# Performance work log

Measured on AMD Instinct MI355X. Metric: run time of the kernel, lower is better.

## Reference

```python
import jax, jax.numpy as jnp
import numpy as np

N0, N1, N2, N3 = 8192, 32768, 65536, 65536
CUM = (N0, N0 + N1, N0 + N1 + N2, N0 + N1 + N2 + N3)  # nodes through hop k
NTOT = CUM[3]
EH = (131072, 262144, 262144)                          # edges per hop (per edge type)
ECUM = (EH[0], EH[0] + EH[1], EH[0] + EH[1] + EH[2])
ETOT = ECUM[2]
C, H, T = 64, 256, 3
HH = H // 2
B, L = 16, 512  # N0 == B * L: equal-length note sequences per graph
LN_EPS = 1e-5


def _ln(x, w, b):
    m = x.mean(-1, keepdims=True)
    v = x.var(-1, keepdims=True)
    return (x - m) / jnp.sqrt(v + LN_EPS) * w + b


def _seg_mean(msgs, dst, n):
    s = jax.ops.segment_sum(msgs, dst, num_segments=n)
    cnt = jax.ops.segment_sum(jnp.ones(dst.shape, msgs.dtype), dst, num_segments=n)
    return s / jnp.maximum(cnt, 1.0)[:, None]


def _l2(x):
    return x / jnp.maximum(jnp.linalg.norm(x, axis=-1, keepdims=True), 1e-12)


def _gru_dir(x, wih, whh, bih, bhh, reverse):
    # x: [B, Lt, Din]; torch gate order (r, z, n)
    gi = jnp.einsum('bld,gd->blg', x, wih) + bih
    gi = jnp.moveaxis(gi, 1, 0)  # [Lt, B, 3*HH]
    h0 = jnp.zeros((x.shape[0], HH), x.dtype)

    def step(h, g):
        gh = h @ whh.T + bhh
        ir, iz, in_ = jnp.split(g, 3, -1)
        hr, hz, hn = jnp.split(gh, 3, -1)
        r = jax.nn.sigmoid(ir + hr)
        z = jax.nn.sigmoid(iz + hz)
        n = jnp.tanh(in_ + r * hn)
        hnew = (1.0 - z) * n + z * h
        return hnew, hnew

    _, ys = jax.lax.scan(step, h0, gi, reverse=reverse)
    return jnp.moveaxis(ys, 0, 1)  # [B, Lt, HH]


def _bigru(x, wih, whh, bih, bhh):
    f = _gru_dir(x, wih[0], whh[0], bih[0], bhh[0], False)
    bwd = _gru_dir(x, wih[1], whh[1], bih[1], bhh[1], True)
    return jnp.concatenate([f, bwd], -1)


def _forward(x, edge_index, batch_size, sage0_proj_w, sage0_proj_b, sage0_lw, sage0_lb,
             sage0_rw, sage_lw, sage_lb, sage_rw, ln_w, ln_b,
             gru_wih0, gru_whh0, gru_bih0, gru_bhh0,
             gru_wih1, gru_whh1, gru_bih1, gru_bhh1,
             rnn_norm_w, rnn_norm_b, mlp1_w, mlp1_b, mlp_ln_w, mlp_ln_b,
             mlp2_w, mlp2_b, cat_w, cat_b):
    # ---- hybrid GRU branch on seed notes (equal lengths -> pad == reshape) ----
    xs = x[:batch_size].reshape(B, L, C)
    h = _bigru(xs, gru_wih0, gru_whh0, gru_bih0, gru_bhh0)
    h = _bigru(h, gru_wih1, gru_whh1, gru_bih1, gru_bhh1)  # inter-layer dropout: eval mode
    h = _ln(h, rnn_norm_w, rnn_norm_b)
    h = _ln(jax.nn.relu(h @ mlp1_w + mlp1_b), mlp_ln_w, mlp_ln_b) @ mlp2_w + mlp2_b
    x_rnn = h.reshape(batch_size, H)

    # ---- GNN layer 0: SAGEConv(project=True, normalize=True), hetero mean over T types ----
    feat = x
    outs = []
    for t in range(T):
        src, dst = edge_index[t, 0], edge_index[t, 1]
        xp = jax.nn.relu(feat @ sage0_proj_w[t] + sage0_proj_b[t])
        agg = _seg_mean(xp[src], dst, NTOT)
        outs.append(_l2(agg @ sage0_lw[t] + sage0_lb[t] + feat @ sage0_rw[t]))
    feat = sum(outs) / T
    feat = _ln(jax.nn.relu(feat), ln_w[0], ln_b[0])  # dropout: eval mode (identity)

    # ---- layers 1..2 with trim_to_layer: drop last sampled hop each layer ----
    n_layer = (CUM[2], CUM[1])
    e_layer = (ECUM[1], ECUM[0])
    for i in range(2):
        n, e = n_layer[i], e_layer[i]
        feat = feat[:n]
        outs = []
        for t in range(T):
            src, dst = edge_index[t, 0, :e], edge_index[t, 1, :e]
            agg = _seg_mean(feat[src], dst, n)
            outs.append(agg @ sage_lw[i, t] + sage_lb[i, t] + feat @ sage_rw[i, t])
        feat = sum(outs) / T
        if i == 0:
            feat = _ln(jax.nn.relu(feat), ln_w[1], ln_b[1])
    x_gnn = feat[:batch_size]
    return jnp.concatenate([x_rnn, x_gnn], -1) @ cat_w + cat_b


def setup_inputs():
    key = jax.random.key(0)
    ks = iter(jax.random.split(key, 64))

    def nrm(shape, fan_in):
        return jax.random.normal(next(ks), shape, jnp.float32) / float(np.sqrt(fan_in))

    # hop-structured edges: hop k has src < CUM[k+1], dst < CUM[k]
    ei = []
    for t in range(T):
        rows, cols = [], []
        for k in range(3):
            rows.append(jax.random.randint(next(ks), (EH[k],), 0, CUM[k + 1]))
            cols.append(jax.random.randint(next(ks), (EH[k],), 0, CUM[k]))
        ei.append(jnp.stack([jnp.concatenate(rows), jnp.concatenate(cols)]))
    edge_index = jnp.stack(ei).astype(jnp.int32)

    return dict(
        x=jax.random.normal(next(ks), (NTOT, C), jnp.float32),
        edge_index=edge_index,
        batch=(jnp.arange(N0) // L).astype(jnp.int32),
        batch_size=N0,
        sage0_proj_w=nrm((T, C, C), C), sage0_proj_b=jnp.zeros((T, C), jnp.float32),
        sage0_lw=nrm((T, C, H), C), sage0_lb=jnp.zeros((T, H), jnp.float32),
        sage0_rw=nrm((T, C, H), C),
        sage_lw=nrm((2, T, H, H), H), sage_lb=jnp.zeros((2, T, H), jnp.float32),
        sage_rw=nrm((2, T, H, H), H),
        ln_w=jnp.ones((2, H), jnp.float32), ln_b=jnp.zeros((2, H), jnp.float32),
        gru_wih0=nrm((2, 3 * HH, C), C), gru_whh0=nrm((2, 3 * HH, HH), HH),
        gru_bih0=jnp.zeros((2, 3 * HH), jnp.float32), gru_bhh0=jnp.zeros((2, 3 * HH), jnp.float32),
        gru_wih1=nrm((2, 3 * HH, H), H), gru_whh1=nrm((2, 3 * HH, HH), HH),
        gru_bih1=jnp.zeros((2, 3 * HH), jnp.float32), gru_bhh1=jnp.zeros((2, 3 * HH), jnp.float32),
        rnn_norm_w=jnp.ones((H,), jnp.float32), rnn_norm_b=jnp.zeros((H,), jnp.float32),
        mlp1_w=nrm((H, H), H), mlp1_b=jnp.zeros((H,), jnp.float32),
        mlp_ln_w=jnp.ones((H,), jnp.float32), mlp_ln_b=jnp.zeros((H,), jnp.float32),
        mlp2_w=nrm((H, H), H), mlp2_b=jnp.zeros((H,), jnp.float32),
        cat_w=nrm((2 * H, H), 2 * H), cat_b=jnp.zeros((H,), jnp.float32),
    )


def reference(x, edge_index, batch, batch_size, sage0_proj_w, sage0_proj_b, sage0_lw,
              sage0_lb, sage0_rw, sage_lw, sage_lb, sage_rw, ln_w, ln_b,
              gru_wih0, gru_whh0, gru_bih0, gru_bhh0, gru_wih1, gru_whh1, gru_bih1,
              gru_bhh1, rnn_norm_w, rnn_norm_b, mlp1_w, mlp1_b, mlp_ln_w, mlp_ln_b,
              mlp2_w, mlp2_b, cat_w, cat_b):
    # batch encodes 16 equal-length (512) sequences; bincount/pad == reshape above
    return _forward(x, edge_index, batch_size, sage0_proj_w, sage0_proj_b, sage0_lw,
                    sage0_lb, sage0_rw, sage_lw, sage_lb, sage_rw, ln_w, ln_b,
                    gru_wih0, gru_whh0, gru_bih0, gru_bhh0, gru_wih1, gru_whh1,
                    gru_bih1, gru_bhh1, rnn_norm_w, rnn_norm_b, mlp1_w, mlp1_b,
                    mlp_ln_w, mlp_ln_b, mlp2_w, mlp2_b, cat_w, cat_b)
```

## Files before the change

kernel.cpp:

```cpp
#include <hip/hip_runtime.h>
#include <stdint.h>

typedef unsigned short u16;
typedef __attribute__((ext_vector_type(8))) short short8;
typedef __attribute__((ext_vector_type(4))) short short4v;
typedef __attribute__((ext_vector_type(4))) float float4v;

#define DEV static __device__ __forceinline__

DEV float bf2f(u16 u){ union { unsigned int i; float f; } c; c.i = ((unsigned int)u) << 16; return c.f; }
DEV u16 f2bf(float f){ union { float ff; unsigned int i; } c; c.ff = f;
  unsigned int x = c.i; return (u16)((x + 0x7fffu + ((x >> 16) & 1u)) >> 16); }

#define MFMA16(a,b,c) __builtin_amdgcn_mfma_f32_16x16x32_bf16((a),(b),(c),0,0,0)

#define ETOTC  655360
#define TSTRIDE 155648
#define NBINS   466944

__global__ void detect_dtype(const u16* __restrict__ xs, int* __restrict__ flag){
  __shared__ int sh[256];
  int t = threadIdx.x; int cnt = 0;
  for (int i = t; i < 4096; i += 256){
    u16 u = xs[i]; int e = (u >> 7) & 0xff;
    cnt += (u == 0 || (e >= 112 && e <= 143)) ? 1 : 0;
  }
  sh[t] = cnt; __syncthreads();
  for (int d = 128; d; d >>= 1){ if (t < d) sh[t] += sh[t+d]; __syncthreads(); }
  if (t == 0) flag[0] = (sh[0] >= 3686) ? 1 : 0;
}

DEV u16 scrub(u16 v){ int e = (v >> 7) & 0xff; return (e == 0xff) ? (u16)0 : v; }

__global__ void convert_x(const void* __restrict__ xin, const int* __restrict__ flag,
                          u16* __restrict__ out){
  int i = blockIdx.x*256 + threadIdx.x;
  u16 v[4];
  if (flag[0] == 1){
    short4v s = ((const short4v*)xin)[i];
#pragma unroll
    for (int j=0;j<4;j++) v[j] = scrub((u16)s[j]);
  } else {
    float4v f = ((const float4v*)xin)[i];
#pragma unroll
    for (int j=0;j<4;j++) v[j] = scrub(f2bf(f[j]));
  }
  short4v o; o[0]=(short)v[0]; o[1]=(short)v[1]; o[2]=(short)v[2]; o[3]=(short)v[3];
  ((short4v*)out)[i] = o;
}

struct WSrc { const void* p[28]; };
__device__ const int g_wcum[29] = {0,12288,12480,61632,62400,111552,504768,506304,899520,
  900032,900544,949696,1048000,1048768,1049536,1246144,1344448,1345216,1345984,1346240,
  1346496,1412032,1412288,1412544,1412800,1478336,1478592,1609664,1609920};

__global__ void convert_w(WSrc d, const int* __restrict__ flag, u16* __restrict__ out){
  int i = blockIdx.x*256 + threadIdx.x;
  if (i >= 1609920) return;
  int lo = 0, hi = 28;
  while (hi - lo > 1){ int m = (lo+hi) >> 1; if (i >= g_wcum[m]) lo = m; else hi = m; }
  int off = i - g_wcum[lo];
  u16 v = (flag[0] == 1) ? ((const u16*)d.p[lo])[off]
                         : f2bf(((const float*)d.p[lo])[off]);
  out[i] = scrub(v);
}

__global__ void packT(const u16* __restrict__ in, u16* __restrict__ out, int K, int N){
  int i = blockIdx.x*256 + threadIdx.x;
  if (i < K*N){ int n = i / K, k = i - n*K; out[i] = in[(size_t)k*N + n]; }
}

__global__ void pack_lr(const u16* __restrict__ lw, const u16* __restrict__ rw,
                        u16* __restrict__ out, int F){
  int K2 = 2*F; long total = 3L*256*K2;
  long i = (long)blockIdx.x*256 + threadIdx.x;
  if (i < total){
    int k = (int)(i % K2); int n = (int)((i / K2) & 255); int t = (int)(i / ((long)K2*256));
    out[i] = (k < F) ? lw[((size_t)t*F + k)*256 + n]
                     : rw[((size_t)t*F + (k-F))*256 + n];
  }
}

__global__ void hist3(const int* __restrict__ ei, int* __restrict__ cnt){
  int g = blockIdx.x*256 + threadIdx.x;
  int t = g / ETOTC, e = g - t*ETOTC;
  int dst = ei[(size_t)t*2*ETOTC + ETOTC + e];
  int base = t*TSTRIDE;
  atomicAdd(&cnt[base + dst], 1);
  if (e < 393216) atomicAdd(&cnt[base + 106496 + dst], 1);
  if (e < 131072) atomicAdd(&cnt[base + 147456 + dst], 1);
}

__global__ void perm3(const int* __restrict__ ei, const int* __restrict__ off,
                      int* __restrict__ slot, int* __restrict__ srcs){
  int g = blockIdx.x*256 + threadIdx.x;
  int t = g / ETOTC, e = g - t*ETOTC;
  int dst = ei[(size_t)t*2*ETOTC + ETOTC + e];
  int src = ei[(size_t)t*2*ETOTC + e];
  int base = t*TSTRIDE;
  { int b = base + dst; srcs[off[b] + atomicAdd(&slot[b], 1)] = src; }
  if (e < 393216){ int b = base + 106496 + dst;
    srcs[off[b] + atomicAdd(&slot[b], 1)] = src; }
  if (e < 131072){ int b = base + 147456 + dst;
    srcs[off[b] + atomicAdd(&slot[b], 1)] = src; }
}

__global__ void scan_blocks(const int* __restrict__ cnt, int* __restrict__ off,
                            int* __restrict__ bsum, int n){
  __shared__ int sh[256];
  int t = threadIdx.x;
  int base = blockIdx.x*2048 + t*8;
  int v[8]; int tot = 0;
#pragma unroll
  for (int j=0;j<8;j++){ v[j] = (base+j < n) ? cnt[base+j] : 0; tot += v[j]; }
  sh[t] = tot; __syncthreads();
  for (int d=1; d<256; d<<=1){
    int y = (t>=d) ? sh[t-d] : 0; __syncthreads();
    sh[t] += y; __syncthreads();
  }
  int run = sh[t] - tot;
#pragma unroll
  for (int j=0;j<8;j++){ if (base+j < n) off[base+j] = run; run += v[j]; }
  if (t == 255) bsum[blockIdx.x] = sh[255];
}

__global__ void scan_top(int* __restrict__ bsum, int G){
  __shared__ int sh[256];
  int t = threadIdx.x;
  int v = (t < G) ? bsum[t] : 0;
  sh[t] = v; __syncthreads();
  for (int d=1; d<256; d<<=1){
    int y = (t>=d) ? sh[t-d] : 0; __syncthreads();
    sh[t] += y; __syncthreads();
  }
  if (t < G) bsum[t] = sh[t] - v;
}

__global__ void scan_add(int* __restrict__ off, const int* __restrict__ bsum, int n){
  int add = bsum[blockIdx.x];
  int base = blockIdx.x*2048 + threadIdx.x*8;
#pragma unroll
  for (int j=0;j<8;j++) if (base+j < n) off[base+j] += add;
}

template<int F>
DEV void gather_body(int w, int lane,
    const int* __restrict__ off, const int* __restrict__ cnt, const int* __restrict__ srcs,
    const u16* __restrict__ feat, int ld, u16* __restrict__ out)
{
  int st = off[w], c = cnt[w];
  float sc = 1.f / (float)(c < 1 ? 1 : c);
  if (F == 64) {
    float a = 0.f, b = 0.f;
    int i = 0;
    for (; i + 4 <= c; i += 4){
      int s0 = srcs[st+i], s1 = srcs[st+i+1], s2 = srcs[st+i+2], s3 = srcs[st+i+3];
      u16 u0 = feat[(size_t)s0*ld + lane];
      u16 u1 = feat[(size_t)s1*ld + lane];
      u16 u2 = feat[(size_t)s2*ld + lane];
      u16 u3 = feat[(size_t)s3*ld + lane];
      a += bf2f(u0) + bf2f(u1);
      b += bf2f(u2) + bf2f(u3);
    }
    for (; i < c; ++i){ int s = srcs[st+i]; a += bf2f(feat[(size_t)s*ld + lane]); }
    out[(size_t)w*64 + lane] = f2bf((a + b)*sc);
  } else {
    float a0=0.f,a1=0.f,a2=0.f,a3=0.f;
    float b0=0.f,b1=0.f,b2=0.f,b3=0.f;
    int i = 0;
    for (; i + 4 <= c; i += 4){
      int s0 = srcs[st+i], s1 = srcs[st+i+1], s2 = srcs[st+i+2], s3 = srcs[st+i+3];
      short4v u0 = *(const short4v*)(feat + (size_t)s0*ld + lane*4);
      short4v u1 = *(const short4v*)(feat + (size_t)s1*ld + lane*4);
      short4v u2 = *(const short4v*)(feat + (size_t)s2*ld + lane*4);
      short4v u3 = *(const short4v*)(feat + (size_t)s3*ld + lane*4);
      a0 += bf2f((u16)u0[0]) + bf2f((u16)u1[0]);
      a1 += bf2f((u16)u0[1]) + bf2f((u16)u1[1]);
      a2 += bf2f((u16)u0[2]) + bf2f((u16)u1[2]);
      a3 += bf2f((u16)u0[3]) + bf2f((u16)u1[3]);
      b0 += bf2f((u16)u2[0]) + bf2f((u16)u3[0]);
      b1 += bf2f((u16)u2[1]) + bf2f((u16)u3[1]);
      b2 += bf2f((u16)u2[2]) + bf2f((u16)u3[2]);
      b3 += bf2f((u16)u2[3]) + bf2f((u16)u3[3]);
    }
    for (; i < c; ++i){
      int s = srcs[st+i];
      short4v u = *(const short4v*)(feat + (size_t)s*ld + lane*4);
      a0 += bf2f((u16)u[0]); a1 += bf2f((u16)u[1]);
      a2 += bf2f((u16)u[2]); a3 += bf2f((u16)u[3]);
    }
    u16* o = out + (size_t)w*256 + lane*4;
    o[0]=f2bf((a0+b0)*sc); o[1]=f2bf((a1+b1)*sc);
    o[2]=f2bf((a2+b2)*sc); o[3]=f2bf((a3+b3)*sc);
  }
}

template<int F>
__global__ __launch_bounds__(256,4) void gather_mean(
    const int* __restrict__ off, const int* __restrict__ cnt, const int* __restrict__ srcs,
    const u16* __restrict__ feat, int ld, u16* __restrict__ out, int rows)
{
  int w = blockIdx.x*4 + (threadIdx.x >> 6);
  int lane = threadIdx.x & 63;
  if (w >= rows) return;
  gather_body<F>(w, lane, off, cnt, srcs, feat, ld, out);
}

__global__ __launch_bounds__(256,2) void ln_rows(
    const u16* __restrict__ in, u16* __restrict__ out,
    const u16* __restrict__ w, const u16* __restrict__ b, int rows)
{
  int r = blockIdx.x*4 + (threadIdx.x >> 6);
  int lane = threadIdx.x & 63;
  if (r >= rows) return;
  short4v u = *(const short4v*)(in + (size_t)r*256 + lane*4);
  float v[4];
#pragma unroll
  for (int i=0;i<4;i++) v[i] = bf2f((u16)u[i]);
  float s = v[0]+v[1]+v[2]+v[3];
  float q = v[0]*v[0]+v[1]*v[1]+v[2]*v[2]+v[3]*v[3];
#pragma unroll
  for (int d=1; d<64; d<<=1){ s += __shfl_xor(s, d); q += __shfl_xor(q, d); }
  float mu = s * (1.f/256.f);
  float var = fmaxf(q * (1.f/256.f) - mu*mu, 0.f);
  float rs = rsqrtf(var + 1e-5f);
  u16* o = out + (size_t)r*256 + lane*4;
#pragma unroll
  for (int i=0;i<4;i++){
    int col = lane*4 + i;
    o[i] = f2bf((v[i]-mu)*rs*bf2f(w[col]) + bf2f(b[col]));
  }
}

#define LGKM0_SB do{ asm volatile("s_waitcnt lgkmcnt(0)" ::: "memory"); \
                     __builtin_amdgcn_sched_barrier(0); \
                     __builtin_amdgcn_s_barrier(); \
                     __builtin_amdgcn_sched_barrier(0); }while(0)

#define GRU_STEP(S, C0, C1, C2) do{                                          \
    const int l_ = dir ? (511 - (S)) : (S);                                  \
    short8 afr_[4];                                                          \
    _Pragma("unroll")                                                        \
    for (int kt=0; kt<4; kt++) afr_[kt] = *(const short8*)(&hbf[kt*32 + lg*8]); \
    float4v acc_[4];                                                         \
    _Pragma("unroll")                                                        \
    for (int nt=0; nt<4; nt++) acc_[nt] = (float4v){0.f,0.f,0.f,0.f};        \
    _Pragma("unroll")                                                        \
    for (int kt=0; kt<4; kt++){                                              \
      _Pragma("unroll")                                                      \
      for (int nt=0; nt<4; nt++) acc_[nt] = MFMA16(afr_[kt], bfrag[nt][kt], acc_[nt]); } \
    if (lane < 16){                                                          \
      _Pragma("unroll")                                                      \
      for (int nt=0; nt<4; nt++) ghs[64*w + nt*16 + lane] = acc_[nt][0];     \
    }                                                                        \
    LGKM0_SB;                                                                \
    if (tid < 128){                                                          \
      float ghr = ghs[tid]       + bhr;                                      \
      float ghz = ghs[128 + tid] + bhz;                                      \
      float ghn = ghs[256 + tid] + bhn;                                      \
      float r_ = 1.f/(1.f + __expf(-((C0) + ghr)));                          \
      float z_ = 1.f/(1.f + __expf(-((C1) + ghz)));                          \
      float xn_ = (C2) + r_*ghn;                                             \
      float th_ = 1.f - 2.f/(__expf(2.f*xn_) + 1.f);                         \
      hreg = (1.f - z_)*th_ + z_*hreg;                                       \
      u16 hb_ = f2bf(hreg);                                                  \
      hbf[tid] = hb_;                                                        \
      hout[((size_t)(b*512 + l_))*256 + dir*128 + tid] = hb_;                \
      int sn_ = (S) + 2;                                                     \
      if (sn_ < 512){                                                        \
        int ln2_ = dir ? (511 - sn_) : sn_;                                  \
        const float* g_ = gbase + (size_t)ln2_*768;                          \
        (C0) = g_[0]; (C1) = g_[128]; (C2) = g_[256];                        \
      }                                                                      \
    }                                                                        \
    LGKM0_SB;                                                                \
  }while(0)

DEV void gru_body(const float* __restrict__ gi, const u16* __restrict__ whh,
                  const u16* __restrict__ bhh, u16* __restrict__ hout,
                  int bid, u16* hbf, float* ghs)
{
  const int b = bid >> 1, dir = bid & 1;
  const int tid = threadIdx.x;
  const int w = tid >> 6, lane = tid & 63;
  const int lr = lane & 15, lg = lane >> 4;

  short8 bfrag[4][4];
#pragma unroll
  for (int nt=0; nt<4; nt++)
#pragma unroll
    for (int kt=0; kt<4; kt++){
      int n = 64*w + nt*16 + lr;
      bfrag[nt][kt] = *(const short8*)(whh + ((size_t)(dir*384 + n))*128 + kt*32 + lg*8);
    }

  const float* gbase = gi + (size_t)b*512*768 + dir*384 + tid;
  float hreg = 0.f, bhr = 0.f, bhz = 0.f, bhn = 0.f;
  float a0=0.f,a1=0.f,a2=0.f, e0=0.f,e1=0.f,e2=0.f;
  if (tid < 128){
    bhr = bf2f(bhh[dir*384 + tid]);
    bhz = bf2f(bhh[dir*384 + 128 + tid]);
    bhn = bf2f(bhh[dir*384 + 256 + tid]);
    const float* g0 = gbase + (size_t)(dir ? 511 : 0)*768;
    a0 = g0[0]; a1 = g0[128]; a2 = g0[256];
    const float* g1 = gbase + (size_t)(dir ? 510 : 1)*768;
    e0 = g1[0]; e1 = g1[128]; e2 = g1[256];
  }
  if (tid < 64) ((unsigned int*)hbf)[tid] = 0u;
  LGKM0_SB;

  for (int s2 = 0; s2 < 512; s2 += 2){
    GRU_STEP(s2,     a0, a1, a2);
    GRU_STEP(s2 + 1, e0, e1, e2);
  }
}

template<int F>
__global__ __launch_bounds__(384,1) void fused_gru_gather(
    const float* __restrict__ gi, const u16* __restrict__ whh,
    const u16* __restrict__ bhh, u16* __restrict__ hout,
    const int* __restrict__ off0, const int* __restrict__ cnt0, const int* __restrict__ srcs,
    const u16* __restrict__ feat, int ld, int featstep,
    u16* __restrict__ aggout, long aggstride, int rows, int bpt)
{
  __shared__ u16 hbf[128];
  __shared__ float ghs[384];
  if (blockIdx.x < 32){
    gru_body(gi, whh, bhh, hout, blockIdx.x, hbf, ghs);
    return;
  }
  int gb = blockIdx.x - 32;
  int t = gb / bpt, rb = gb - t*bpt;
  int w = rb*6 + (threadIdx.x >> 6);
  int lane = threadIdx.x & 63;
  if (w >= rows) return;
  gather_body<F>(w, lane, off0 + t*TSTRIDE, cnt0 + t*TSTRIDE, srcs,
                 feat + (size_t)t*featstep, ld, aggout + (size_t)t*aggstride);
}

template<int EPI, bool OUTF32>
__global__ __launch_bounds__(256,1) void gemm_bt(
    const u16* __restrict__ A, int lda,
    const u16* __restrict__ WT, int K, int N,
    const u16* __restrict__ bias,
    const u16* __restrict__ lnw, const u16* __restrict__ lnb,
    void* __restrict__ Cp, int ldc, const int* __restrict__ dynof)
{
  __shared__ u16 As[64*72];
  __shared__ u16 Bs[256*72];
  __shared__ float redS[4][64];
  __shared__ float redQ[4][64];
  __shared__ float muL[64], rsL[64];
  const int tid = threadIdx.x;
  const int lane = tid & 63, wid = tid >> 6;
  const int lr = lane & 15, lg = lane >> 4;
  const int m0 = blockIdx.x * 64;
  const int col0 = blockIdx.y * 256;
  float4v acc[4][4];
#pragma unroll
  for (int i=0;i<4;i++)
#pragma unroll
    for (int j=0;j<4;j++) acc[i][j] = (float4v){0.f,0.f,0.f,0.f};

  for (int k0 = 0; k0 < K; k0 += 64){
#pragma unroll
    for (int v = 0; v < 2; v++){
      int idx = tid + v*256; int r = idx >> 3, c8 = (idx & 7) << 3;
      *(short8*)(&As[r*72 + c8]) = *(const short8*)(A + (size_t)(m0+r)*lda + k0 + c8);
    }
#pragma unroll
    for (int v = 0; v < 8; v++){
      int idx = tid + v*256; int nn = idx >> 3, c8 = (idx & 7) << 3;
      short8 val = {0,0,0,0,0,0,0,0};
      if (col0 + nn < N) val = *(const short8*)(WT + (size_t)(col0+nn)*K + k0 + c8);
      *(short8*)(&Bs[nn*72 + c8]) = val;
    }
    __syncthreads();
#pragma unroll
    for (int kk = 0; kk < 2; kk++){
      short8 af[4], bfr[4];
#pragma unroll
      for (int i=0;i<4;i++) af[i]  = *(const short8*)(&As[(16*i+lr)*72 + kk*32 + lg*8]);
#pragma unroll
      for (int j=0;j<4;j++) bfr[j] = *(const short8*)(&Bs[(wid*64+16*j+lr)*72 + kk*32 + lg*8]);
#pragma unroll
      for (int i=0;i<4;i++)
#pragma unroll
        for (int j=0;j<4;j++) acc[i][j] = MFMA16(af[i], bfr[j], acc[i][j]);
    }
    __syncthreads();
  }
  int cols[4];
#pragma unroll
  for (int j=0;j<4;j++) cols[j] = col0 + wid*64 + 16*j + lr;
#pragma unroll
  for (int j=0;j<4;j++){
    float bv = (cols[j] < N) ? bf2f(bias[cols[j]]) : 0.f;
#pragma unroll
    for (int i=0;i<4;i++)
#pragma unroll
      for (int r=0;r<4;r++) acc[i][j][r] += bv;
  }
  if (EPI >= 1){
#pragma unroll
    for (int i=0;i<4;i++)
#pragma unroll
      for (int j=0;j<4;j++)
#pragma unroll
        for (int r=0;r<4;r++) acc[i][j][r] = fmaxf(acc[i][j][r], 0.f);
  }
  if (EPI == 2){
#pragma unroll
    for (int i=0;i<4;i++)
#pragma unroll
      for (int r=0;r<4;r++){
        float p = acc[i][0][r]+acc[i][1][r]+acc[i][2][r]+acc[i][3][r];
        float q = acc[i][0][r]*acc[i][0][r]+acc[i][1][r]*acc[i][1][r]
                 +acc[i][2][r]*acc[i][2][r]+acc[i][3][r]*acc[i][3][r];
#pragma unroll
        for (int d=1; d<16; d<<=1){ p += __shfl_xor(p,d); q += __shfl_xor(q,d); }
        if (lr == 0){ redS[wid][16*i + lg*4 + r] = p; redQ[wid][16*i + lg*4 + r] = q; }
      }
    __syncthreads();
    if (tid < 64){
      float s = redS[0][tid]+redS[1][tid]+redS[2][tid]+redS[3][tid];
      float q = redQ[0][tid]+redQ[1][tid]+redQ[2][tid]+redQ[3][tid];
      float mu = s * (1.f/256.f);
      float var = fmaxf(q * (1.f/256.f) - mu*mu, 0.f);
      muL[tid] = mu; rsL[tid] = rsqrtf(var + 1e-5f);
    }
    __syncthreads();
#pragma unroll
    for (int i=0;i<4;i++)
#pragma unroll
      for (int r=0;r<4;r++){
        int rl = 16*i + lg*4 + r;
        float mu = muL[rl], rs = rsL[rl];
#pragma unroll
        for (int j=0;j<4;j++){
          float w = bf2f(lnw[cols[j]]), bb = bf2f(lnb[cols[j]]);
          acc[i][j][r] = (acc[i][j][r]-mu)*rs*w + bb;
        }
      }
  }
  bool of32 = OUTF32;
  if (dynof) of32 = (dynof[0] == 0);
#pragma unroll
  for (int i=0;i<4;i++)
#pragma unroll
    for (int r=0;r<4;r++){
      int row = m0 + 16*i + lg*4 + r;
#pragma unroll
      for (int j=0;j<4;j++) if (cols[j] < N){
        if (of32) ((float*)Cp)[(size_t)row*ldc + cols[j]] = acc[i][j][r];
        else ((u16*)Cp)[(size_t)row*ldc + cols[j]] = f2bf(acc[i][j][r]);
      }
    }
}

template<int F, bool DO_L2, bool DO_LN>
__global__ __launch_bounds__(256,1) void sage_fused(
    const u16* __restrict__ A1, long a1t, const u16* __restrict__ A2, int lda2,
    const u16* __restrict__ WTp, const u16* __restrict__ lbp,
    const u16* __restrict__ lnw, const u16* __restrict__ lnb,
    u16* __restrict__ out, int ldc, int outcol)
{
  constexpr int K2 = 2*F;
  __shared__ u16 As[64*72];
  __shared__ u16 Bs[256*72];
  __shared__ float redS[4][64];
  __shared__ float redQ[4][64];
  __shared__ float rowA[64], rowB[64];
  const int tid = threadIdx.x;
  const int lane = tid & 63, wid = tid >> 6;
  const int lr = lane & 15, lg = lane >> 4;
  const int m0 = blockIdx.x * 64;
  int colsL[4];
#pragma unroll
  for (int j=0;j<4;j++) colsL[j] = wid*64 + 16*j + lr;
  float4v facc[4][4];
#pragma unroll
  for (int i=0;i<4;i++)
#pragma unroll
    for (int j=0;j<4;j++) facc[i][j] = (float4v){0.f,0.f,0.f,0.f};

  for (int t=0; t<3; ++t){
    float4v acc[4][4];
#pragma unroll
    for (int i=0;i<4;i++)
#pragma unroll
      for (int j=0;j<4;j++) acc[i][j] = (float4v){0.f,0.f,0.f,0.f};
    const u16* WT  = WTp + (size_t)t*256*K2;
    const u16* A1b = A1 + (size_t)t*a1t;
    for (int k0 = 0; k0 < K2; k0 += 64){
      const u16* Ab; int la, kb;
      if (k0 < F){ Ab = A1b; la = F; kb = k0; } else { Ab = A2; la = lda2; kb = k0 - F; }
#pragma unroll
      for (int v=0; v<2; v++){
        int idx = tid + v*256; int r = idx >> 3, c8 = (idx & 7) << 3;
        *(short8*)(&As[r*72 + c8]) = *(const short8*)(Ab + (size_t)(m0+r)*la + kb + c8);
      }
#pragma unroll
      for (int v=0; v<8; v++){
        int idx = tid + v*256; int nn = idx >> 3, c8 = (idx & 7) << 3;
        *(short8*)(&Bs[nn*72 + c8]) = *(const short8*)(WT + (size_t)nn*K2 + k0 + c8);
      }
      __syncthreads();
#pragma unroll
      for (int kk = 0; kk < 2; kk++){
        short8 af[4], bfr[4];
#pragma unroll
        for (int i=0;i<4;i++) af[i]  = *(const short8*)(&As[(16*i+lr)*72 + kk*32 + lg*8]);
#pragma unroll
        for (int j=0;j<4;j++) bfr[j] = *(const short8*)(&Bs[(wid*64+16*j+lr)*72 + kk*32 + lg*8]);
#pragma unroll
        for (int i=0;i<4;i++)
#pragma unroll
          for (int j=0;j<4;j++) acc[i][j] = MFMA16(af[i], bfr[j], acc[i][j]);
      }
      __syncthreads();
    }
#pragma unroll
    for (int j=0;j<4;j++){
      float bv = bf2f(lbp[t*256 + colsL[j]]);
#pragma unroll
      for (int i=0;i<4;i++)
#pragma unroll
        for (int r=0;r<4;r++) acc[i][j][r] += bv;
    }
    if (DO_L2){
#pragma unroll
      for (int i=0;i<4;i++)
#pragma unroll
        for (int r=0;r<4;r++){
          float q = acc[i][0][r]*acc[i][0][r]+acc[i][1][r]*acc[i][1][r]
                   +acc[i][2][r]*acc[i][2][r]+acc[i][3][r]*acc[i][3][r];
#pragma unroll
          for (int d=1; d<16; d<<=1) q += __shfl_xor(q,d);
          if (lr == 0) redQ[wid][16*i + lg*4 + r] = q;
        }
      __syncthreads();
      if (tid < 64){
        float q = redQ[0][tid]+redQ[1][tid]+redQ[2][tid]+redQ[3][tid];
        rowA[tid] = 1.f / fmaxf(sqrtf(q), 1e-12f);
      }
      __syncthreads();
#pragma unroll
      for (int i=0;i<4;i++)
#pragma unroll
        for (int r=0;r<4;r++){
          float sc = rowA[16*i + lg*4 + r];
#pragma unroll
          for (int j=0;j<4;j++) acc[i][j][r] *= sc;
        }
      __syncthreads();
    }
#pragma unroll
    for (int i=0;i<4;i++)
#pragma unroll
      for (int j=0;j<4;j++)
#pragma unroll
        for (int r=0;r<4;r++) facc[i][j][r] += acc[i][j][r];
  }
  const float inv3 = (1.f/3.f);
#pragma unroll
  for (int i=0;i<4;i++)
#pragma unroll
    for (int j=0;j<4;j++)
#pragma unroll
      for (int r=0;r<4;r++) facc[i][j][r] *= inv3;
  if (DO_LN){
#pragma unroll
    for (int i=0;i<4;i++)
#pragma unroll
      for (int j=0;j<4;j++)
#pragma unroll
        for (int r=0;r<4;r++) facc[i][j][r] = fmaxf(facc[i][j][r], 0.f);
#pragma unroll
    for (int i=0;i<4;i++)
#pragma unroll
      for (int r=0;r<4;r++){
        float p = facc[i][0][r]+facc[i][1][r]+facc[i][2][r]+facc[i][3][r];
        float q = facc[i][0][r]*facc[i][0][r]+facc[i][1][r]*facc[i][1][r]
                 +facc[i][2][r]*facc[i][2][r]+facc[i][3][r]*facc[i][3][r];
#pragma unroll
        for (int d=1; d<16; d<<=1){ p += __shfl_xor(p,d); q += __shfl_xor(q,d); }
        if (lr == 0){ redS[wid][16*i + lg*4 + r] = p; redQ[wid][16*i + lg*4 + r] = q; }
      }
    __syncthreads();
    if (tid < 64){
      float s = redS[0][tid]+redS[1][tid]+redS[2][tid]+redS[3][tid];
      float q = redQ[0][tid]+redQ[1][tid]+redQ[2][tid]+redQ[3][tid];
      float mu = s * (1.f/256.f);
      float var = fmaxf(q * (1.f/256.f) - mu*mu, 0.f);
      rowA[tid] = mu; rowB[tid] = rsqrtf(var + 1e-5f);
    }
    __syncthreads();
#pragma unroll
    for (int i=0;i<4;i++)
#pragma unroll
      for (int r=0;r<4;r++){
        int rl = 16*i + lg*4 + r;
        float mu = rowA[rl], rs = rowB[rl];
#pragma unroll
        for (int j=0;j<4;j++){
          float w = bf2f(lnw[colsL[j]]), bb = bf2f(lnb[colsL[j]]);
          facc[i][j][r] = (facc[i][j][r]-mu)*rs*w + bb;
        }
      }
  }
#pragma unroll
  for (int i=0;i<4;i++)
#pragma unroll
    for (int r=0;r<4;r++){
      int row = m0 + 16*i + lg*4 + r;
#pragma unroll
      for (int j=0;j<4;j++)
        out[(size_t)row*ldc + outcol + colsL[j]] = f2bf(facc[i][j][r]);
    }
}

extern "C" void kernel_launch(void* const* d_in, const int* in_sizes, int n_in,
                              void* d_out, int out_size, void* d_ws, size_t ws_size,
                              hipStream_t stream)
{
  (void)in_sizes; (void)n_in; (void)out_size;
  const int* ei = (const int*)d_in[1];

  char* ws = (char*)d_ws;
  size_t o = 0;
  auto alloc = [&](size_t b){ size_t p = o; o += (b + 255) & ~(size_t)255; return p; };
  char* RA   = ws + alloc(66060288);
  u16* XP3   = (u16*)RA;
  u16* AGGB1 = (u16*)RA;
  char* RR   = ws + alloc(41943040);
  float* GI  = (float*)RR;
  u16* H0    = (u16*)(RR + 25165824);
  u16* H1    = (u16*)(RR + 29360128);
  u16* HA    = (u16*)(RR + 33554432);
  u16* HB    = (u16*)(RR + 37748736);
  char* RB   = ws + alloc(40894464);
  u16* AGGB0 = (u16*)RB;
  u16* AGGB2 = (u16*)RB;
  u16* FEAT2 = (u16*)(RB + 12582912);
  u16* FEAT  = (u16*)(ws + alloc(106496ull*256*2));
  u16* CAT   = (u16*)(ws + alloc(8192ull*512*2));
  u16* AR    = (u16*)(ws + alloc(12619968ull*2));
  u16* WXP   = (u16*)(ws + alloc(192ull*64*2));
  u16* WP0   = (u16*)(ws + alloc(3ull*256*128*2));
  u16* WP1   = (u16*)(ws + alloc(3ull*256*512*2));
  u16* WP2   = (u16*)(ws + alloc(3ull*256*512*2));
  u16* M1T   = (u16*)(ws + alloc(256ull*256*2));
  u16* M2T   = (u16*)(ws + alloc(256ull*256*2));
  u16* CTT   = (u16*)(ws + alloc(256ull*512*2));
  int* CNT   = (int*)(ws + alloc((size_t)NBINS*4));
  int* OFF   = (int*)(ws + alloc((size_t)NBINS*4));
  int* SLOT  = (int*)(ws + alloc((size_t)NBINS*4));
  int* BSUM  = (int*)(ws + alloc(256ull*4));
  int* SRCS  = (int*)(ws + alloc(3538944ull*4));
  int* FLAG  = (int*)(ws + alloc(256));
  if (o > ws_size) return;

  u16* x16    = AR;
  u16* projw6 = AR + 11010048; u16* projb6 = AR + 11022336;
  u16* s0lw6  = AR + 11022528; u16* s0lb6  = AR + 11071680; u16* s0rw6 = AR + 11072448;
  u16* slw6   = AR + 11121600; u16* slb6   = AR + 11514816; u16* srw6  = AR + 11516352;
  u16* lnw6   = AR + 11909568; u16* lnb6   = AR + 11910080;
  u16* wih0b  = AR + 11910592; u16* whh0b  = AR + 11959744;
  u16* bih0b  = AR + 12058048; u16* bhh0b  = AR + 12058816;
  u16* wih1b  = AR + 12059584; u16* whh1b  = AR + 12256192;
  u16* bih1b  = AR + 12354496; u16* bhh1b  = AR + 12355264;
  u16* rnw6   = AR + 12356032; u16* rnb6   = AR + 12356288;
  u16* mlp1w6 = AR + 12356544; u16* mlp1b6 = AR + 12422080;
  u16* mlnw6  = AR + 12422336; u16* mlnb6  = AR + 12422592;
  u16* mlp2w6 = AR + 12422848; u16* mlp2b6 = AR + 12488384;
  u16* catw6  = AR + 12488640; u16* catb6  = AR + 12619712;

  detect_dtype<<<dim3(1),dim3(256),0,stream>>>((const u16*)d_in[0], FLAG);
  convert_x<<<dim3(10752),dim3(256),0,stream>>>(d_in[0], FLAG, x16);
  WSrc wsrc;
  for (int i=0;i<28;i++) wsrc.p[i] = d_in[4+i];
  convert_w<<<dim3(6289),dim3(256),0,stream>>>(wsrc, FLAG, AR + 11010048);

  packT<<<dim3(256),dim3(256),0,stream>>>(mlp1w6, M1T, 256, 256);
  packT<<<dim3(256),dim3(256),0,stream>>>(mlp2w6, M2T, 256, 256);
  packT<<<dim3(512),dim3(256),0,stream>>>(catw6,  CTT, 512, 256);
  for (int t=0;t<3;t++)
    packT<<<dim3(16),dim3(256),0,stream>>>(projw6 + (size_t)t*4096, WXP + (size_t)t*4096, 64, 64);
  pack_lr<<<dim3(384),dim3(256),0,stream>>>(s0lw6, s0rw6, WP0, 64);
  pack_lr<<<dim3(1536),dim3(256),0,stream>>>(slw6,               srw6,               WP1, 256);
  pack_lr<<<dim3(1536),dim3(256),0,stream>>>(slw6 + 3ull*256*256, srw6 + 3ull*256*256, WP2, 256);

  hipMemsetAsync(CNT, 0, (size_t)NBINS*4, stream);
  hist3<<<dim3(7680),dim3(256),0,stream>>>(ei, CNT);
  scan_blocks<<<dim3(228),dim3(256),0,stream>>>(CNT, OFF, BSUM, NBINS);
  scan_top<<<dim3(1),dim3(256),0,stream>>>(BSUM, 228);
  scan_add<<<dim3(228),dim3(256),0,stream>>>(OFF, BSUM, NBINS);
  hipMemsetAsync(SLOT, 0, (size_t)NBINS*4, stream);
  perm3<<<dim3(7680),dim3(256),0,stream>>>(ei, OFF, SLOT, SRCS);

  gemm_bt<0,true><<<dim3(128,3),dim3(256),0,stream>>>(x16, 64, wih0b, 64, 768, bih0b, nullptr, nullptr, GI, 768, nullptr);
  gemm_bt<1,false><<<dim3(2688,1),dim3(256),0,stream>>>(x16, 64, WXP, 64, 192, projb6, nullptr, nullptr, XP3, 192, nullptr);

  fused_gru_gather<64><<<dim3(32 + 3*17750),dim3(384),0,stream>>>(
      GI, whh0b, bhh0b, H0,
      OFF, CNT, SRCS, XP3, 192, 64, AGGB0, (long)106496*64, 106496, 17750);

  gemm_bt<0,true><<<dim3(128,3),dim3(256),0,stream>>>(H0, 256, wih1b, 256, 768, bih1b, nullptr, nullptr, GI, 768, nullptr);
  sage_fused<64,true,true><<<dim3(1664),dim3(256),0,stream>>>(
      AGGB0, (long)106496*64, x16, 64, WP0, s0lb6, lnw6, lnb6, FEAT, 256, 0);

  fused_gru_gather<256><<<dim3(32 + 3*6827),dim3(384),0,stream>>>(
      GI, whh1b, bhh1b, H1,
      OFF + 106496, CNT + 106496, SRCS, FEAT, 256, 0, AGGB1, (long)40960*256, 40960, 6827);

  sage_fused<256,false,true><<<dim3(640),dim3(256),0,stream>>>(
      AGGB1, (long)40960*256, FEAT, 256, WP1, slb6, lnw6+256, lnb6+256, FEAT2, 256, 0);
  for (int t=0;t<3;t++)
    gather_mean<256><<<dim3(2048),dim3(256),0,stream>>>(
        OFF + t*TSTRIDE + 147456, CNT + t*TSTRIDE + 147456, SRCS, FEAT2, 256,
        AGGB2 + (size_t)t*8192*256, 8192);
  sage_fused<256,false,false><<<dim3(128),dim3(256),0,stream>>>(
      AGGB2, (long)8192*256, FEAT2, 256, WP2, slb6 + 3*256, nullptr, nullptr, CAT, 512, 256);

  ln_rows<<<dim3(2048),dim3(256),0,stream>>>(H1, HA, rnw6, rnb6, 8192);
  gemm_bt<2,false><<<dim3(128,1),dim3(256),0,stream>>>(HA, 256, M1T, 256, 256, mlp1b6, mlnw6, mlnb6, HB, 256, nullptr);
  gemm_bt<0,false><<<dim3(128,1),dim3(256),0,stream>>>(HB, 256, M2T, 256, 256, mlp2b6, nullptr, nullptr, CAT, 512, nullptr);

  gemm_bt<0,false><<<dim3(128,1),dim3(256),0,stream>>>(CAT, 512, CTT, 512, 256, catb6,
      nullptr, nullptr, d_out, 256, FLAG);
}
```

Before: 1.526 ms.

## Merge independent GEMM, SAGE, LN and gather launches into horizontally fused kernels

Independent stages (GRU input GEMM with SAGE layer 0, SAGE layer 1 with the RNN LayerNorm, MLP1 with the layer-2 gathers, MLP2 with SAGE layer 2) are combined into single launches that pick their role from the block index, using one shared-memory struct. This is meant to cut launch overhead and fill the GPU with concurrent work from independent branches. It also raises the GRU recurrence wave priority so co-resident gather blocks do not delay the serial critical path. The risks are that gather and LN blocks now run under the 256-thread, 1-block launch bounds and reserve the full GEMM shared memory, which may lower their occupancy.

```diff
diff --git a/kernel.cpp b/kernel.cpp
--- a/kernel.cpp
+++ b/kernel.cpp
@@ -17,6 +17,14 @@
 #define ETOTC  655360
 #define TSTRIDE 155648
 #define NBINS   466944
+
+struct SM {
+  u16 As[64*72];
+  u16 Bs[256*72];
+  float redS[4][64];
+  float redQ[4][64];
+  float rowA[64], rowB[64];
+};
 
 __global__ void detect_dtype(const u16* __restrict__ xs, int* __restrict__ flag){
   __shared__ int sh[256];
@@ -195,24 +203,10 @@
   }
 }
 
-template<int F>
-__global__ __launch_bounds__(256,4) void gather_mean(
-    const int* __restrict__ off, const int* __restrict__ cnt, const int* __restrict__ srcs,
-    const u16* __restrict__ feat, int ld, u16* __restrict__ out, int rows)
-{
-  int w = blockIdx.x*4 + (threadIdx.x >> 6);
-  int lane = threadIdx.x & 63;
-  if (w >= rows) return;
-  gather_body<F>(w, lane, off, cnt, srcs, feat, ld, out);
-}
-
-__global__ __launch_bounds__(256,2) void ln_rows(
+DEV void ln_body(int r, int lane,
     const u16* __restrict__ in, u16* __restrict__ out,
-    const u16* __restrict__ w, const u16* __restrict__ b, int rows)
-{
-  int r = blockIdx.x*4 + (threadIdx.x >> 6);
-  int lane = threadIdx.x & 63;
-  if (r >= rows) return;
+    const u16* __restrict__ w, const u16* __restrict__ b)
+{
   short4v u = *(const short4v*)(in + (size_t)r*256 + lane*4);
   float v[4];
 #pragma unroll
@@ -309,10 +303,12 @@
   if (tid < 64) ((unsigned int*)hbf)[tid] = 0u;
   LGKM0_SB;
 
+  __builtin_amdgcn_s_setprio(1);
   for (int s2 = 0; s2 < 512; s2 += 2){
     GRU_STEP(s2,     a0, a1, a2);
     GRU_STEP(s2 + 1, e0, e1, e2);
   }
+  __builtin_amdgcn_s_setprio(0);
 }
 
 template<int F>
@@ -339,6 +335,122 @@
 }
 
 template<int EPI, bool OUTF32>
+DEV void gemm_body(SM& sm, int bx, int by,
+    const u16* __restrict__ A, int lda,
+    const u16* __restrict__ WT, int K, int N,
+    const u16* __restrict__ bias,
+    const u16* __restrict__ lnw, const u16* __restrict__ lnb,
+    void* __restrict__ Cp, int ldc, const int* __restrict__ dynof)
+{
+  u16* As = sm.As; u16* Bs = sm.Bs;
+  const int tid = threadIdx.x;
+  const int lane = tid & 63, wid = tid >> 6;
+  const int lr = lane & 15, lg = lane >> 4;
+  const int m0 = bx * 64;
+  const int col0 = by * 256;
+  float4v acc[4][4];
+#pragma unroll
+  for (int i=0;i<4;i++)
+#pragma unroll
+    for (int j=0;j<4;j++) acc[i][j] = (float4v){0.f,0.f,0.f,0.f};
+
+  for (int k0 = 0; k0 < K; k0 += 64){
+#pragma unroll
+    for (int v = 0; v < 2; v++){
+      int idx = tid + v*256; int r = idx >> 3, c8 = (idx & 7) << 3;
+      *(short8*)(&As[r*72 + c8]) = *(const short8*)(A + (size_t)(m0+r)*lda + k0 + c8);
+    }
+#pragma unroll
+    for (int v = 0; v < 8; v++){
+      int idx = tid + v*256; int nn = idx >> 3, c8 = (idx & 7) << 3;
+      short8 val = {0,0,0,0,0,0,0,0};
+      if (col0 + nn < N) val = *(const short8*)(WT + (size_t)(col0+nn)*K + k0 + c8);
+      *(short8*)(&Bs[nn*72 + c8]) = val;
+    }
+    __syncthreads();
+#pragma unroll
+    for (int kk = 0; kk < 2; kk++){
+      short8 af[4], bfr[4];
+#pragma unroll
+      for (int i=0;i<4;i++) af[i]  = *(const short8*)(&As[(16*i+lr)*72 + kk*32 + lg*8]);
+#pragma unroll
+      for (int j=0;j<4;j++) bfr[j] = *(const short8*)(&Bs[(wid*64+16*j+lr)*72 + kk*32 + lg*8]);
+#pragma unroll
+      for (int i=0;i<4;i++)
+#pragma unroll
+        for (int j=0;j<4;j++) acc[i][j] = MFMA16(af[i], bfr[j], acc[i][j]);
+    }
+    __syncthreads();
+  }
+  int cols[4];
+#pragma unroll
+  for (int j=0;j<4;j++) cols[j] = col0 + wid*64 + 16*j + lr;
+#pragma unroll
+  for (int j=0;j<4;j++){
+    float bv = (cols[j] < N) ? bf2f(bias[cols[j]]) : 0.f;
+#pragma unroll
+    for (int i=0;i<4;i++)
+#pragma unroll
+      for (int r=0;r<4;r++) acc[i][j][r] += bv;
+  }
+  if (EPI >= 1){
+#pragma unroll
+    for (int i=0;i<4;i++)
+#pragma unroll
+      for (int j=0;j<4;j++)
+#pragma unroll
+        for (int r=0;r<4;r++) acc[i][j][r] = fmaxf(acc[i][j][r], 0.f);
+  }
+  if (EPI == 2){
+#pragma unroll
+    for (int i=0;i<4;i++)
+#pragma unroll
+      for (int r=0;r<4;r++){
+        float p = acc[i][0][r]+acc[i][1][r]+acc[i][2][r]+acc[i][3][r];
+        float q = acc[i][0][r]*acc[i][0][r]+acc[i][1][r]*acc[i][1][r]
+                 +acc[i][2][r]*acc[i][2][r]+acc[i][3][r]*acc[i][3][r];
+#pragma unroll
+        for (int d=1; d<16; d<<=1){ p += __shfl_xor(p,d); q += __shfl_xor(q,d); }
+        if (lr == 0){ sm.redS[wid][16*i + lg*4 + r] = p; sm.redQ[wid][16*i + lg*4 + r] = q; }
+      }
+    __syncthreads();
+    if (tid < 64){
+      float s = sm.redS[0][tid]+sm.redS[1][tid]+sm.redS[2][tid]+sm.redS[3][tid];
+      float q = sm.redQ[0][tid]+sm.redQ[1][tid]+sm.redQ[2][tid]+sm.redQ[3][tid];
+      float mu = s * (1.f/256.f);
+      float var = fmaxf(q * (1.f/256.f) - mu*mu, 0.f);
+      sm.rowA[tid] = mu; sm.rowB[tid] = rsqrtf(var + 1e-5f);
+    }
+    __syncthreads();
+#pragma unroll
+    for (int i=0;i<4;i++)
+#pragma unroll
+      for (int r=0;r<4;r++){
+        int rl = 16*i + lg*4 + r;
+        float mu = sm.rowA[rl], rs = sm.rowB[rl];
+#pragma unroll
+        for (int j=0;j<4;j++){
+          float w = bf2f(lnw[cols[j]]), bb = bf2f(lnb[cols[j]]);
+          acc[i][j][r] = (acc[i][j][r]-mu)*rs*w + bb;
+        }
+      }
+  }
+  bool of32 = OUTF32;
+  if (dynof) of32 = (dynof[0] == 0);
+#pragma unroll
+  for (int i=0;i<4;i++)
+#pragma unroll
+    for (int r=0;r<4;r++){
+      int row = m0 + 16*i + lg*4 + r;
+#pragma unroll
+      for (int j=0;j<4;j++) if (cols[j] < N){
+        if (of32) ((float*)Cp)[(size_t)row*ldc + cols[j]] = acc[i][j][r];
+        else ((u16*)Cp)[(size_t)row*ldc + cols[j]] = f2bf(acc[i][j][r]);
+      }
+    }
+}
+
+template<int EPI, bool OUTF32>
 __global__ __launch_bounds__(256,1) void gemm_bt(
     const u16* __restrict__ A, int lda,
     const u16* __restrict__ WT, int K, int N,
@@ -346,135 +458,23 @@
     const u16* __restrict__ lnw, const u16* __restrict__ lnb,
     void* __restrict__ Cp, int ldc, const int* __restrict__ dynof)
 {
-  __shared__ u16 As[64*72];
-  __shared__ u16 Bs[256*72];
-  __shared__ float redS[4][64];
-  __shared__ float redQ[4][64];
-  __shared__ float muL[64], rsL[64];
-  const int tid = threadIdx.x;
-  const int lane = tid & 63, wid = tid >> 6;
-  const int lr = lane & 15, lg = lane >> 4;
-  const int m0 = blockIdx.x * 64;
-  const int col0 = blockIdx.y * 256;
-  float4v acc[4][4];
-#pragma unroll
-  for (int i=0;i<4;i++)
-#pragma unroll
-    for (int j=0;j<4;j++) acc[i][j] = (float4v){0.f,0.f,0.f,0.f};
-
-  for (int k0 = 0; k0 < K; k0 += 64){
-#pragma unroll
-    for (int v = 0; v < 2; v++){
-      int idx = tid + v*256; int r = idx >> 3, c8 = (idx & 7) << 3;
-      *(short8*)(&As[r*72 + c8]) = *(const short8*)(A + (size_t)(m0+r)*lda + k0 + c8);
-    }
-#pragma unroll
-    for (int v = 0; v < 8; v++){
-      int idx = tid + v*256; int nn = idx >> 3, c8 = (idx & 7) << 3;
-      short8 val = {0,0,0,0,0,0,0,0};
-      if (col0 + nn < N) val = *(const short8*)(WT + (size_t)(col0+nn)*K + k0 + c8);
-      *(short8*)(&Bs[nn*72 + c8]) = val;
-    }
-    __syncthreads();
-#pragma unroll
-    for (int kk = 0; kk < 2; kk++){
-      short8 af[4], bfr[4];
-#pragma unroll
-      for (int i=0;i<4;i++) af[i]  = *(const short8*)(&As[(16*i+lr)*72 + kk*32 + lg*8]);
-#pragma unroll
-      for (int j=0;j<4;j++) bfr[j] = *(const short8*)(&Bs[(wid*64+16*j+lr)*72 + kk*32 + lg*8]);
-#pragma unroll
-      for (int i=0;i<4;i++)
-#pragma unroll
-        for (int j=0;j<4;j++) acc[i][j] = MFMA16(af[i], bfr[j], acc[i][j]);
-    }
-    __syncthreads();
-  }
-  int cols[4];
-#pragma unroll
-  for (int j=0;j<4;j++) cols[j] = col0 + wid*64 + 16*j + lr;
-#pragma unroll
-  for (int j=0;j<4;j++){
-    float bv = (cols[j] < N) ? bf2f(bias[cols[j]]) : 0.f;
-#pragma unroll
-    for (int i=0;i<4;i++)
-#pragma unroll
-      for (int r=0;r<4;r++) acc[i][j][r] += bv;
-  }
-  if (EPI >= 1){
-#pragma unroll
-    for (int i=0;i<4;i++)
-#pragma unroll
-      for (int j=0;j<4;j++)
-#pragma unroll
-        for (int r=0;r<4;r++) acc[i][j][r] = fmaxf(acc[i][j][r], 0.f);
-  }
-  if (EPI == 2){
-#pragma unroll
-    for (int i=0;i<4;i++)
-#pragma unroll
-      for (int r=0;r<4;r++){
-        float p = acc[i][0][r]+acc[i][1][r]+acc[i][2][r]+acc[i][3][r];
-        float q = acc[i][0][r]*acc[i][0][r]+acc[i][1][r]*acc[i][1][r]
-                 +acc[i][2][r]*acc[i][2][r]+acc[i][3][r]*acc[i][3][r];
-#pragma unroll
-        for (int d=1; d<16; d<<=1){ p += __shfl_xor(p,d); q += __shfl_xor(q,d); }
-        if (lr == 0){ redS[wid][16*i + lg*4 + r] = p; redQ[wid][16*i + lg*4 + r] = q; }
-      }
-    __syncthreads();
-    if (tid < 64){
-      float s = redS[0][tid]+redS[1][tid]+redS[2][tid]+redS[3][tid];
-      float q = redQ[0][tid]+redQ[1][tid]+redQ[2][tid]+redQ[3][tid];
-      float mu = s * (1.f/256.f);
-      float var = fmaxf(q * (1.f/256.f) - mu*mu, 0.f);
-      muL[tid] = mu; rsL[tid] = rsqrtf(var + 1e-5f);
-    }
-    __syncthreads();
-#pragma unroll
-    for (int i=0;i<4;i++)
-#pragma unroll
-      for (int r=0;r<4;r++){
-        int rl = 16*i + lg*4 + r;
-        float mu = muL[rl], rs = rsL[rl];
-#pragma unroll
-        for (int j=0;j<4;j++){
-          float w = bf2f(lnw[cols[j]]), bb = bf2f(lnb[cols[j]]);
-          acc[i][j][r] = (acc[i][j][r]-mu)*rs*w + bb;
-        }
-      }
-  }
-  bool of32 = OUTF32;
-  if (dynof) of32 = (dynof[0] == 0);
-#pragma unroll
-  for (int i=0;i<4;i++)
-#pragma unroll
-    for (int r=0;r<4;r++){
-      int row = m0 + 16*i + lg*4 + r;
-#pragma unroll
-      for (int j=0;j<4;j++) if (cols[j] < N){
-        if (of32) ((float*)Cp)[(size_t)row*ldc + cols[j]] = acc[i][j][r];
-        else ((u16*)Cp)[(size_t)row*ldc + cols[j]] = f2bf(acc[i][j][r]);
-      }
-    }
+  __shared__ SM sm;
+  gemm_body<EPI,OUTF32>(sm, blockIdx.x, blockIdx.y, A, lda, WT, K, N, bias, lnw, lnb, Cp, ldc, dynof);
 }
 
 template<int F, bool DO_L2, bool DO_LN>
-__global__ __launch_bounds__(256,1) void sage_fused(
+DEV void sage_body(SM& sm, int bx,
     const u16* __restrict__ A1, long a1t, const u16* __restrict__ A2, int lda2,
     const u16* __restrict__ WTp, const u16* __restrict__ lbp,
     const u16* __restrict__ lnw, const u16* __restrict__ lnb,
     u16* __restrict__ out, int ldc, int outcol)
 {
   constexpr int K2 = 2*F;
-  __shared__ u16 As[64*72];
-  __shared__ u16 Bs[256*72];
-  __shared__ float redS[4][64];
-  __shared__ float redQ[4][64];
-  __shared__ float rowA[64], rowB[64];
+  u16* As = sm.As; u16* Bs = sm.Bs;
   const int tid = threadIdx.x;
   const int lane = tid & 63, wid = tid >> 6;
   const int lr = lane & 15, lg = lane >> 4;
-  const int m0 = blockIdx.x * 64;
+  const int m0 = bx * 64;
   int colsL[4];
 #pragma unroll
   for (int j=0;j<4;j++) colsL[j] = wid*64 + 16*j + lr;
@@ -537,19 +537,19 @@
                    +acc[i][2][r]*acc[i][2][r]+acc[i][3][r]*acc[i][3][r];
 #pragma unroll
           for (int d=1; d<16; d<<=1) q += __shfl_xor(q,d);
-          if (lr == 0) redQ[wid][16*i + lg*4 + r] = q;
+          if (lr == 0) sm.redQ[wid][16*i + lg*4 + r] = q;
         }
       __syncthreads();
       if (tid < 64){
-        float q = redQ[0][tid]+redQ[1][tid]+redQ[2][tid]+redQ[3][tid];
-        rowA[tid] = 1.f / fmaxf(sqrtf(q), 1e-12f);
+        float q = sm.redQ[0][tid]+sm.redQ[1][tid]+sm.redQ[2][tid]+sm.redQ[3][tid];
+        sm.rowA[tid] = 1.f / fmaxf(sqrtf(q), 1e-12f);
       }
       __syncthreads();
 #pragma unroll
       for (int i=0;i<4;i++)
 #pragma unroll
         for (int r=0;r<4;r++){
-          float sc = rowA[16*i + lg*4 + r];
+          float sc = sm.rowA[16*i + lg*4 + r];
 #pragma unroll
           for (int j=0;j<4;j++) acc[i][j][r] *= sc;
         }
@@ -585,15 +585,15 @@
                  +facc[i][2][r]*facc[i][2][r]+facc[i][3][r]*facc[i][3][r];
 #pragma unroll
         for (int d=1; d<16; d<<=1){ p += __shfl_xor(p,d); q += __shfl_xor(q,d); }
-        if (lr == 0){ redS[wid][16*i + lg*4 + r] = p; redQ[wid][16*i + lg*4 + r] = q; }
+        if (lr == 0){ sm.redS[wid][16*i + lg*4 + r] = p; sm.redQ[wid][16*i + lg*4 + r] = q; }
       }
     __syncthreads();
     if (tid < 64){
-      float s = redS[0][tid]+redS[1][tid]+redS[2][tid]+redS[3][tid];
-      float q = redQ[0][tid]+redQ[1][tid]+redQ[2][tid]+redQ[3][tid];
+      float s = sm.redS[0][tid]+sm.redS[1][tid]+sm.redS[2][tid]+sm.redS[3][tid];
+      float q = sm.redQ[0][tid]+sm.redQ[1][tid]+sm.redQ[2][tid]+sm.redQ[3][tid];
       float mu = s * (1.f/256.f);
       float var = fmaxf(q * (1.f/256.f) - mu*mu, 0.f);
-      rowA[tid] = mu; rowB[tid] = rsqrtf(var + 1e-5f);
+      sm.rowA[tid] = mu; sm.rowB[tid] = rsqrtf(var + 1e-5f);
     }
     __syncthreads();
 #pragma unroll
@@ -601,7 +601,7 @@
 #pragma unroll
       for (int r=0;r<4;r++){
         int rl = 16*i + lg*4 + r;
-        float mu = rowA[rl], rs = rowB[rl];
+        float mu = sm.rowA[rl], rs = sm.rowB[rl];
 #pragma unroll
         for (int j=0;j<4;j++){
           float w = bf2f(lnw[colsL[j]]), bb = bf2f(lnb[colsL[j]]);
@@ -618,6 +618,77 @@
       for (int j=0;j<4;j++)
         out[(size_t)row*ldc + outcol + colsL[j]] = f2bf(facc[i][j][r]);
     }
+}
+
+__global__ __launch_bounds__(256,1) void fused_gemm_sage0(
+    const u16* __restrict__ H0, const u16* __restrict__ wih1b, const u16* __restrict__ bih1b,
+    float* __restrict__ GI,
+    const u16* __restrict__ AGGB0, const u16* __restrict__ x16, const u16* __restrict__ WP0,
+    const u16* __restrict__ s0lb, const u16* __restrict__ lnw, const u16* __restrict__ lnb,
+    u16* __restrict__ FEAT)
+{
+  __shared__ SM sm;
+  int b = blockIdx.x;
+  if (b < 384)
+    gemm_body<0,true>(sm, b & 127, b >> 7, H0, 256, wih1b, 256, 768, bih1b,
+                      nullptr, nullptr, GI, 768, nullptr);
+  else
+    sage_body<64,true,true>(sm, b - 384, AGGB0, (long)106496*64, x16, 64, WP0, s0lb,
+                            lnw, lnb, FEAT, 256, 0);
+}
+
+__global__ __launch_bounds__(256,1) void fused_ln_sage1(
+    const u16* __restrict__ AGGB1, const u16* __restrict__ FEAT, const u16* __restrict__ WP1,
+    const u16* __restrict__ slb, const u16* __restrict__ lnw, const u16* __restrict__ lnb,
+    u16* __restrict__ FEAT2,
+    const u16* __restrict__ H1, u16* __restrict__ HA,
+    const u16* __restrict__ rnw, const u16* __restrict__ rnb)
+{
+  __shared__ SM sm;
+  int b = blockIdx.x;
+  if (b < 640)
+    sage_body<256,false,true>(sm, b, AGGB1, (long)40960*256, FEAT, 256, WP1, slb,
+                              lnw, lnb, FEAT2, 256, 0);
+  else {
+    int r = (b - 640)*4 + (threadIdx.x >> 6);
+    ln_body(r, threadIdx.x & 63, H1, HA, rnw, rnb);
+  }
+}
+
+__global__ __launch_bounds__(256,1) void fused_mlp1_gather2(
+    const u16* __restrict__ HA, const u16* __restrict__ M1T, const u16* __restrict__ mlp1b,
+    const u16* __restrict__ mlnw, const u16* __restrict__ mlnb, u16* __restrict__ HB,
+    const int* __restrict__ OFF, const int* __restrict__ CNT, const int* __restrict__ SRCS,
+    const u16* __restrict__ FEAT2, u16* __restrict__ AGGB2)
+{
+  __shared__ SM sm;
+  int b = blockIdx.x;
+  if (b < 128){
+    gemm_body<2,false>(sm, b, 0, HA, 256, M1T, 256, 256, mlp1b, mlnw, mlnb, HB, 256, nullptr);
+  } else {
+    int g = b - 128;
+    int t = g / 2048, rb = g - t*2048;
+    int w = rb*4 + (threadIdx.x >> 6);
+    int lane = threadIdx.x & 63;
+    if (w < 8192)
+      gather_body<256>(w, lane, OFF + t*TSTRIDE + 147456, CNT + t*TSTRIDE + 147456, SRCS,
+                       FEAT2, 256, AGGB2 + (size_t)t*8192*256);
+  }
+}
+
+__global__ __launch_bounds__(256,1) void fused_mlp2_sage2(
+    const u16* __restrict__ HB, const u16* __restrict__ M2T, const u16* __restrict__ mlp2b,
+    u16* __restrict__ CAT,
+    const u16* __restrict__ AGGB2, const u16* __restrict__ FEAT2, const u16* __restrict__ WP2,
+    const u16* __restrict__ slb2)
+{
+  __shared__ SM sm;
+  int b = blockIdx.x;
+  if (b < 128)
+    gemm_body<0,false>(sm, b, 0, HB, 256, M2T, 256, 256, mlp2b, nullptr, nullptr, CAT, 512, nullptr);
+  else
+    sage_body<256,false,false>(sm, b - 128, AGGB2, (long)8192*256, FEAT2, 256, WP2, slb2,
+                               nullptr, nullptr, CAT, 512, 256);
 }
 
 extern "C" void kernel_launch(void* const* d_in, const int* in_sizes, int n_in,
@@ -706,26 +777,25 @@
       GI, whh0b, bhh0b, H0,
       OFF, CNT, SRCS, XP3, 192, 64, AGGB0, (long)106496*64, 106496, 17750);
 
-  gemm_bt<0,true><<<dim3(128,3),dim3(256),0,stream>>>(H0, 256, wih1b, 256, 768, bih1b, nullptr, nullptr, GI, 768, nullptr);
-  sage_fused<64,true,true><<<dim3(1664),dim3(256),0,stream>>>(
-      AGGB0, (long)106496*64, x16, 64, WP0, s0lb6, lnw6, lnb6, FEAT, 256, 0);
+  fused_gemm_sage0<<<dim3(2048),dim3(256),0,stream>>>(
+      H0, wih1b, bih1b, GI,
+      AGGB0, x16, WP0, s0lb6, lnw6, lnb6, FEAT);
 
   fused_gru_gather<256><<<dim3(32 + 3*6827),dim3(384),0,stream>>>(
       GI, whh1b, bhh1b, H1,
       OFF + 106496, CNT + 106496, SRCS, FEAT, 256, 0, AGGB1, (long)40960*256, 40960, 6827);
 
-  sage_fused<256,false,true><<<dim3(640),dim3(256),0,stream>>>(
-      AGGB1, (long)40960*256, FEAT, 256, WP1, slb6, lnw6+256, lnb6+256, FEAT2, 256, 0);
-  for (int t=0;t<3;t++)
-    gather_mean<256><<<dim3(2048),dim3(256),0,stream>>>(
-        OFF + t*TSTRIDE + 147456, CNT + t*TSTRIDE + 147456, SRCS, FEAT2, 256,
-        AGGB2 + (size_t)t*8192*256, 8192);
-  sage_fused<256,false,false><<<dim3(128),dim3(256),0,stream>>>(
-      AGGB2, (long)8192*256, FEAT2, 256, WP2, slb6 + 3*256, nullptr, nullptr, CAT, 512, 256);
-
-  ln_rows<<<dim3(2048),dim3(256),0,stream>>>(H1, HA, rnw6, rnb6, 8192);
-  gemm_bt<2,false><<<dim3(128,1),dim3(256),0,stream>>>(HA, 256, M1T, 256, 256, mlp1b6, mlnw6, mlnb6, HB, 256, nullptr);
-  gemm_bt<0,false><<<dim3(128,1),dim3(256),0,stream>>>(HB, 256, M2T, 256, 256, mlp2b6, nullptr, nullptr, CAT, 512, nullptr);
+  fused_ln_sage1<<<dim3(2688),dim3(256),0,stream>>>(
+      AGGB1, FEAT, WP1, slb6, lnw6+256, lnb6+256, FEAT2,
+      H1, HA, rnw6, rnb6);
+
+  fused_mlp1_gather2<<<dim3(6272),dim3(256),0,stream>>>(
+      HA, M1T, mlp1b6, mlnw6, mlnb6, HB,
+      OFF, CNT, SRCS, FEAT2, AGGB2);
+
+  fused_mlp2_sage2<<<dim3(256),dim3(256),0,stream>>>(
+      HB, M2T, mlp2b6, CAT,
+      AGGB2, FEAT2, WP2, slb6 + 3*256);
 
   gemm_bt<0,false><<<dim3(128,1),dim3(256),0,stream>>>(CAT, 512, CTT, 512, 256, catb6,
       nullptr, nullptr, d_out, 256, FLAG);
```

New measurement: 1.586 ms. 3.9% more time.
